# Kernel optimization log

Hardware: AMD Instinct MI355X
Metric: run time of the kernel (lower is better)

## Reference

```python
import jax, jax.numpy as jnp
import numpy as np

N_NODES = 100000
N_EDGES = 1600000
D_IN = 128
UNITS = 128


def setup_inputs() -> dict:
    key = jax.random.key(0)
    k1, k2, k3, k4, k5 = jax.random.split(key, 5)
    x = jax.random.normal(k1, (N_NODES, D_IN), dtype=jnp.float32)
    # glorot-uniform-like dense weight
    limit = float(np.sqrt(6.0 / (D_IN + UNITS)))
    w = jax.random.uniform(k2, (D_IN, UNITS), minval=-limit, maxval=limit, dtype=jnp.float32)
    # COO sparse adjacency: A[row, col] = val
    edge_row = jax.random.randint(k3, (N_EDGES,), 0, N_NODES, dtype=jnp.int32)
    edge_col = jax.random.randint(k4, (N_EDGES,), 0, N_NODES, dtype=jnp.int32)
    edge_val = jax.random.uniform(k5, (N_EDGES,), dtype=jnp.float32)
    return {"x": x, "w": w, "edge_row": edge_row, "edge_col": edge_col, "edge_val": edge_val}


def reference(x, w, edge_row, edge_col, edge_val):
    # dropout rate = 0.0 -> identity (module default)
    xw = x @ w                                   # [N, units] dense projection
    # sparse adjacency propagation: out[i] = sum_e val[e] * xw[col[e]] for row[e]==i
    msgs = xw[edge_col] * edge_val[:, None]      # [E, units] irregular gather
    out = jax.ops.segment_sum(msgs, edge_row, num_segments=x.shape[0])
    return jax.nn.relu(out)                      # activation
```

## Files before the change

### kernel.cpp

```cpp
#include <hip/hip_runtime.h>

#define N_NODES 100000
#define N_EDGES 1600000
#define D 128
#define NB 512
#define BCAP 3584
#define BSTRIDE 16
#define CHUNK 4000
#define NSCAT 400
#define NGEMMB 512
#define NTILES 1563
#define HCAP 1792

typedef __attribute__((ext_vector_type(8))) short  short8;
typedef __attribute__((ext_vector_type(4))) float  floatx4;

__device__ __forceinline__ ushort f2bf(float f) {
    unsigned u = __float_as_uint(f);
    u += 0x7FFF + ((u >> 16) & 1);
    return (ushort)(u >> 16);
}
__device__ __forceinline__ float bf2f(ushort s) {
    return __uint_as_float((unsigned)s << 16);
}
__device__ __forceinline__ int bucket_of(int r)  { return (int)(((unsigned)r << 9) / 100000u); }
__device__ __forceinline__ int row_start(int b)  { return (b * 100000 + 511) >> 9; }

union SMem {
    struct {
        int2  stage[CHUNK];
        int   sA[NB];
        int   sB[NB];
        int   lcur[NB];
        int   gbase[NB];
        short sbuck[CHUNK];
    } sc;
    struct {
        ushort wt[128 * 128];
        ushort ct[4][16 * 128];
    } ge;
};

__global__ __launch_bounds__(256) void gemm_and_scatter(const float* __restrict__ x,
                                                        const float* __restrict__ w,
                                                        ushort* __restrict__ xwb,
                                                        const int* __restrict__ erow,
                                                        const int* __restrict__ ecol,
                                                        const float* __restrict__ eval,
                                                        int* __restrict__ bcnt,
                                                        int2* __restrict__ bkt) {
    __shared__ SMem sm;
    const int t = threadIdx.x;

    if (blockIdx.x < NGEMMB) {
        ushort* wt = sm.ge.wt;
        const int wv   = t >> 6;
        const int lane = t & 63;
        const int m    = lane & 15;
        const int q    = lane >> 4;

        {
            const float4* w4 = (const float4*)w;
            for (int i = t; i < 4096; i += 256) {
                const float4 v = w4[i];
                const int k = i >> 5;
                const int n = (i & 31) << 2;
                const int c = k >> 3, kc = k & 7;
#pragma unroll
                for (int d = 0; d < 4; ++d) {
                    const float val = (d == 0) ? v.x : (d == 1) ? v.y : (d == 2) ? v.z : v.w;
                    const int nn = n + d;
                    wt[(nn << 7) | (((c ^ (nn & 15)) & 15) << 3) | kc] = f2bf(val);
                }
            }
        }
        __syncthreads();

        for (int tb = blockIdx.x; tb < NTILES; tb += NGEMMB) {
            const int rbase = tb * 64 + wv * 16;
            if (rbase >= N_NODES) break;

            const float* xrow = x + (size_t)min(rbase + m, N_NODES - 1) * D;

            floatx4 acc[8];
#pragma unroll
            for (int tt = 0; tt < 8; ++tt) acc[tt] = (floatx4){0.f, 0.f, 0.f, 0.f};

#pragma unroll
            for (int kk = 0; kk < D; kk += 32) {
                const float4 a0 = *(const float4*)(xrow + kk + q * 8);
                const float4 a1 = *(const float4*)(xrow + kk + q * 8 + 4);
                short8 a;
                a[0] = (short)f2bf(a0.x); a[1] = (short)f2bf(a0.y);
                a[2] = (short)f2bf(a0.z); a[3] = (short)f2bf(a0.w);
                a[4] = (short)f2bf(a1.x); a[5] = (short)f2bf(a1.y);
                a[6] = (short)f2bf(a1.z); a[7] = (short)f2bf(a1.w);

#pragma unroll
                for (int tt = 0; tt < 8; ++tt) {
                    const int n  = tt * 16 + m;
                    const int cc = (((kk >> 3) + q) ^ m) & 15;
                    const short8 b = *(const short8*)&wt[(n << 7) | (cc << 3)];
                    acc[tt] = __builtin_amdgcn_mfma_f32_16x16x32_bf16(a, b, acc[tt], 0, 0, 0);
                }
            }

#pragma unroll
            for (int tt = 0; tt < 8; ++tt) {
#pragma unroll
                for (int r = 0; r < 4; ++r) {
                    sm.ge.ct[wv][((q << 2) | r) * 128 + tt * 16 + m] = f2bf(acc[tt][r]);
                }
            }
            const int rl  = lane >> 2;
            const int ch  = lane & 3;
            const int row = rbase + rl;
            if (row < N_NODES) {
                const ushort* srcp = &sm.ge.ct[wv][rl * 128 + ch * 32];
                ushort*       dstp = &xwb[(size_t)row * D + ch * 32];
#pragma unroll
                for (int u = 0; u < 4; ++u) {
                    ((int4*)dstp)[u] = ((const int4*)srcp)[u];
                }
            }
        }
    } else {
        const int e0 = (blockIdx.x - NGEMMB) * CHUNK;
        int*   sA    = sm.sc.sA;
        int*   sB    = sm.sc.sB;
        int*   lcur  = sm.sc.lcur;
        int*   gbase = sm.sc.gbase;
        short* sbuck = sm.sc.sbuck;
        int2*  stage = sm.sc.stage;

        sA[t] = 0; sA[t + 256] = 0;
        __syncthreads();

        for (int i = t; i < CHUNK; i += 256) {
            atomicAdd(&sA[bucket_of(erow[e0 + i])], 1);
        }
        __syncthreads();

        int cur = 0;
        int* bufs[2] = {sA, sB};
#pragma unroll
        for (int o = 1; o < 512; o <<= 1) {
            const int* src = bufs[cur];
            int*       dst = bufs[cur ^ 1];
            const int i0 = t, i1 = t + 256;
            dst[i0] = src[i0] + ((i0 >= o) ? src[i0 - o] : 0);
            dst[i1] = src[i1] + ((i1 >= o) ? src[i1 - o] : 0);
            cur ^= 1;
            __syncthreads();
        }
        {
            const int* incl = bufs[cur];
            int*       excl = bufs[cur ^ 1];
            excl[t]       = (t == 0) ? 0 : incl[t - 1];
            excl[t + 256] = incl[t + 255];
        }
        __syncthreads();
        int* L = bufs[cur ^ 1];

        for (int b = t; b < NB; b += 256) {
            lcur[b] = L[b];
            const int cnt = ((b == NB - 1) ? CHUNK : L[b + 1]) - L[b];
            gbase[b] = (cnt > 0) ? atomicAdd(&bcnt[b * BSTRIDE], cnt) : 0;
        }
        __syncthreads();

        for (int i = t; i < CHUNK; i += 256) {
            const int   r = erow[e0 + i];
            const int   c = ecol[e0 + i];
            const float v = eval[e0 + i];
            const int   b = bucket_of(r);
            const int  rl = r - row_start(b);
            const int pos = atomicAdd(&lcur[b], 1);
            stage[pos] = make_int2((rl << 17) | c, __float_as_int(v));
            sbuck[pos] = (short)b;
        }
        __syncthreads();

        for (int i = t; i < CHUNK; i += 256) {
            const int b   = sbuck[i];
            const int dst = gbase[b] + (i - L[b]);
            if (dst < BCAP) bkt[(size_t)b * BCAP + dst] = stage[i];
        }
    }
}

__global__ __launch_bounds__(256, 4) void csr_gather(const int* __restrict__ bcnt,
                                                     const int2* __restrict__ bkt,
                                                     const ushort* __restrict__ xwb,
                                                     float* __restrict__ out) {
    __shared__ int2 lcsr[HCAP];
    __shared__ int  sA[256], sB[256], lcur[256];
    const int bg = blockIdx.x;
    const int b  = bg >> 1;
    const int h  = bg & 1;
    const int t  = threadIdx.x;
    const int n  = min(bcnt[b * BSTRIDE], BCAP);
    const int r0    = row_start(b);
    const int nrows = row_start(b + 1) - r0;
    const int mid   = (nrows + 1) >> 1;
    const int lo    = h ? mid : 0;
    const int hi    = h ? nrows : mid;
    const int nloc  = hi - lo;

    const int2* src = bkt + (size_t)b * BCAP;
    sA[t] = 0;
    __syncthreads();

    for (int i = t; i < n; i += 256) {
        const int rl = (int)(((unsigned)src[i].x) >> 17);
        if (rl >= lo && rl < hi) atomicAdd(&sA[rl - lo], 1);
    }
    __syncthreads();

    int cur = 0;
    int* bufs[2] = {sA, sB};
#pragma unroll
    for (int o = 1; o < 256; o <<= 1) {
        const int* s = bufs[cur];
        int*       d = bufs[cur ^ 1];
        d[t] = s[t] + ((t >= o) ? s[t - o] : 0);
        cur ^= 1;
        __syncthreads();
    }
    lcur[t] = (t == 0) ? 0 : bufs[cur][t - 1];
    __syncthreads();

    for (int i = t; i < n; i += 256) {
        const int2 e = src[i];
        const int rl = (int)(((unsigned)e.x) >> 17);
        if (rl >= lo && rl < hi) {
            const int pos = atomicAdd(&lcur[rl - lo], 1);
            if (pos < HCAP) lcsr[pos] = make_int2(e.x & 0x1FFFF, e.y);
        }
    }
    __syncthreads();

    const int qid = t >> 4;
    const int lc  = (t & 15) << 3;

    for (int ln = qid; ln < nloc; ln += 16) {
        int start = (ln == 0) ? 0 : lcur[ln - 1];
        int end   = lcur[ln];
        start = min(start, HCAP);
        end   = min(end, HCAP);

        float acc[8] = {0, 0, 0, 0, 0, 0, 0, 0};

        for (int j = start; j < end; j += 4) {
            const int jb = j + 1, jc = j + 2, jd = j + 3;
            const int2 e0 = lcsr[j];
            const int2 e1 = lcsr[min(jb, end - 1)];
            const int2 e2 = lcsr[min(jc, end - 1)];
            const int2 e3 = lcsr[min(jd, end - 1)];
            const short8 m0 = *(const short8*)&xwb[(size_t)e0.x * D + lc];
            const short8 m1 = *(const short8*)&xwb[(size_t)e1.x * D + lc];
            const short8 m2 = *(const short8*)&xwb[(size_t)e2.x * D + lc];
            const short8 m3 = *(const short8*)&xwb[(size_t)e3.x * D + lc];
            const float v0 = __int_as_float(e0.y);
            const float v1 = (jb < end) ? __int_as_float(e1.y) : 0.f;
            const float v2 = (jc < end) ? __int_as_float(e2.y) : 0.f;
            const float v3 = (jd < end) ? __int_as_float(e3.y) : 0.f;
#pragma unroll
            for (int i = 0; i < 8; ++i) {
                acc[i] += v0 * bf2f((ushort)m0[i]);
                acc[i] += v1 * bf2f((ushort)m1[i]);
                acc[i] += v2 * bf2f((ushort)m2[i]);
                acc[i] += v3 * bf2f((ushort)m3[i]);
            }
        }

        float* o = out + (size_t)(r0 + lo + ln) * D + lc;
        *(float4*)(o + 0) = make_float4(fmaxf(acc[0], 0.f), fmaxf(acc[1], 0.f),
                                        fmaxf(acc[2], 0.f), fmaxf(acc[3], 0.f));
        *(float4*)(o + 4) = make_float4(fmaxf(acc[4], 0.f), fmaxf(acc[5], 0.f),
                                        fmaxf(acc[6], 0.f), fmaxf(acc[7], 0.f));
    }
}

extern "C" void kernel_launch(void* const* d_in, const int* in_sizes, int n_in,
                              void* d_out, int out_size, void* d_ws, size_t ws_size,
                              hipStream_t stream) {
    const float* x    = (const float*)d_in[0];
    const float* w    = (const float*)d_in[1];
    const int*   erow = (const int*)d_in[2];
    const int*   ecol = (const int*)d_in[3];
    const float* eval = (const float*)d_in[4];
    float*       out  = (float*)d_out;

    char*   ws_base = (char*)d_ws;
    ushort* xwb  = (ushort*)ws_base;
    int*    bcnt = (int*)(ws_base + 25600000);
    int2*   bkt  = (int2*)(ws_base + 25632768);

    (void)hipMemsetAsync(bcnt, 0, 32768, stream);

    gemm_and_scatter<<<NGEMMB + NSCAT, 256, 0, stream>>>(x, w, xwb, erow, ecol, eval, bcnt, bkt);
    csr_gather<<<NB * 2, 256, 0, stream>>>(bcnt, bkt, xwb, out);
}
```

Measured before the change: 217.5 us.

## Prefetch next GEMM tile rows into registers and pad output staging stride

```diff
diff --git a/kernel.cpp b/kernel.cpp
--- a/kernel.cpp
+++ b/kernel.cpp
@@ -8,9 +8,10 @@
 #define BSTRIDE 16
 #define CHUNK 4000
 #define NSCAT 400
-#define NGEMMB 512
+#define NGEMMB 521
 #define NTILES 1563
 #define HCAP 1792
+#define CTS 132
 
 typedef __attribute__((ext_vector_type(8))) short  short8;
 typedef __attribute__((ext_vector_type(4))) float  floatx4;
@@ -37,7 +38,7 @@
     } sc;
     struct {
         ushort wt[128 * 128];
-        ushort ct[4][16 * 128];
+        ushort ct[4][16 * CTS];
     } ge;
 };
 
@@ -76,32 +77,56 @@
         }
         __syncthreads();
 
+        float4 xa[8];
+        {
+            const int rb0 = blockIdx.x * 64 + wv * 16;
+            const float* xr = x + (size_t)min(rb0 + m, N_NODES - 1) * D + q * 8;
+#pragma unroll
+            for (int k2 = 0; k2 < 4; ++k2) {
+                xa[k2 * 2 + 0] = *(const float4*)(xr + k2 * 32);
+                xa[k2 * 2 + 1] = *(const float4*)(xr + k2 * 32 + 4);
+            }
+        }
+
         for (int tb = blockIdx.x; tb < NTILES; tb += NGEMMB) {
             const int rbase = tb * 64 + wv * 16;
-            if (rbase >= N_NODES) break;
-
-            const float* xrow = x + (size_t)min(rbase + m, N_NODES - 1) * D;
-
-            floatx4 acc[8];
-#pragma unroll
-            for (int tt = 0; tt < 8; ++tt) acc[tt] = (floatx4){0.f, 0.f, 0.f, 0.f};
-
-#pragma unroll
-            for (int kk = 0; kk < D; kk += 32) {
-                const float4 a0 = *(const float4*)(xrow + kk + q * 8);
-                const float4 a1 = *(const float4*)(xrow + kk + q * 8 + 4);
+
+            short8 afr[4];
+#pragma unroll
+            for (int k2 = 0; k2 < 4; ++k2) {
+                const float4 a0 = xa[k2 * 2 + 0];
+                const float4 a1 = xa[k2 * 2 + 1];
                 short8 a;
                 a[0] = (short)f2bf(a0.x); a[1] = (short)f2bf(a0.y);
                 a[2] = (short)f2bf(a0.z); a[3] = (short)f2bf(a0.w);
                 a[4] = (short)f2bf(a1.x); a[5] = (short)f2bf(a1.y);
                 a[6] = (short)f2bf(a1.z); a[7] = (short)f2bf(a1.w);
-
+                afr[k2] = a;
+            }
+
+            const int tnext = tb + NGEMMB;
+            if (tnext < NTILES) {
+                const int rbn = tnext * 64 + wv * 16;
+                const float* xr = x + (size_t)min(rbn + m, N_NODES - 1) * D + q * 8;
+#pragma unroll
+                for (int k2 = 0; k2 < 4; ++k2) {
+                    xa[k2 * 2 + 0] = *(const float4*)(xr + k2 * 32);
+                    xa[k2 * 2 + 1] = *(const float4*)(xr + k2 * 32 + 4);
+                }
+            }
+
+            floatx4 acc[8];
+#pragma unroll
+            for (int tt = 0; tt < 8; ++tt) acc[tt] = (floatx4){0.f, 0.f, 0.f, 0.f};
+
+#pragma unroll
+            for (int k2 = 0; k2 < 4; ++k2) {
 #pragma unroll
                 for (int tt = 0; tt < 8; ++tt) {
                     const int n  = tt * 16 + m;
-                    const int cc = (((kk >> 3) + q) ^ m) & 15;
+                    const int cc = (((k2 << 2) + q) ^ m) & 15;
                     const short8 b = *(const short8*)&wt[(n << 7) | (cc << 3)];
-                    acc[tt] = __builtin_amdgcn_mfma_f32_16x16x32_bf16(a, b, acc[tt], 0, 0, 0);
+                    acc[tt] = __builtin_amdgcn_mfma_f32_16x16x32_bf16(afr[k2], b, acc[tt], 0, 0, 0);
                 }
             }
 
@@ -109,14 +134,14 @@
             for (int tt = 0; tt < 8; ++tt) {
 #pragma unroll
                 for (int r = 0; r < 4; ++r) {
-                    sm.ge.ct[wv][((q << 2) | r) * 128 + tt * 16 + m] = f2bf(acc[tt][r]);
+                    sm.ge.ct[wv][((q << 2) | r) * CTS + tt * 16 + m] = f2bf(acc[tt][r]);
                 }
             }
             const int rl  = lane >> 2;
             const int ch  = lane & 3;
             const int row = rbase + rl;
             if (row < N_NODES) {
-                const ushort* srcp = &sm.ge.ct[wv][rl * 128 + ch * 32];
+                const ushort* srcp = &sm.ge.ct[wv][rl * CTS + ch * 32];
                 ushort*       dstp = &xwb[(size_t)row * D + ch * 32];
 #pragma unroll
                 for (int u = 0; u < 4; ++u) {
```

New measurement: 215.9 us. About the same (-0.8%).
